# Kernel optimization log

Measured on AMD Instinct MI355X. Metric: run time of the kernel, lower is better.

The kernel has to match this reference:

```python
import jax, jax.numpy as jnp
import numpy as np

B, T, V, C, K = 256, 2048, 128, 512, 10


def setup_inputs() -> dict:
    key = jax.random.key(0)
    k0, k1, k2, k3 = jax.random.split(key, 4)
    x = jax.random.normal(k0, (B, C), dtype=jnp.float32)
    # kappa_old: running attention position, non-negative, somewhere in [0, T)
    kappa_old = jax.random.uniform(k1, (B, K), dtype=jnp.float32) * T
    # onehots: one-hot encoded text, (B, T, V)
    char_ids = jax.random.randint(k2, (B, T), 0, V)
    onehots = jax.nn.one_hot(char_ids, V, dtype=jnp.float32)
    # Linear(cell_size, 3*K) params; torch stores weight as (out, in)
    W = jax.random.normal(k3, (3 * K, C), dtype=jnp.float32) * 0.02
    b = jnp.zeros((3 * K,), dtype=jnp.float32)
    return {"x": x, "kappa_old": kappa_old, "onehots": onehots, "W": W, "b": b}


def reference(x, kappa_old, onehots, W, b):
    max_text_len = onehots.shape[1]
    params = jnp.exp(x @ W.T + b)                      # (B, 3K)
    alpha, beta, pre_kappa = jnp.split(params, 3, axis=-1)  # each (B, K)
    kappa = kappa_old + pre_kappa                      # (B, K)
    indices = jnp.arange(max_text_len, dtype=x.dtype)  # (T,)
    # gravity: (B, K, T) via broadcast, then exp + alpha-weighted reduce over K
    gravity = -beta[:, :, None] * (kappa[:, :, None] - indices) ** 2
    phi = jnp.einsum("bk,bkt->bt", alpha, jnp.exp(gravity))  # (B, T)
    w = jnp.einsum("bt,btv->bv", phi, onehots)               # (B, V)
    return (w, kappa, phi)
```

## Files before the change

kernel.cpp:

```cpp
#include <hip/hip_runtime.h>

#define B_ 256
#define T_ 2048
#define V_ 128
#define C_ 512
#define K_ 10

#define W_OFF 0
#define KAPPA_OFF (B_ * V_)
#define PHI_OFF   (B_ * V_ + B_ * K_)

#define S_ 8
#define TS_ (T_ / S_)

__global__ __launch_bounds__(256) void window_fused(
    const float* __restrict__ x, const float* __restrict__ kappa_old,
    const float* __restrict__ W, const float* __restrict__ bias,
    const float* __restrict__ onehots, float* __restrict__ out) {
  const int s = blockIdx.x;
  const int b = blockIdx.y;
  const int tid = threadIdx.x;

  __shared__ float4 xs4[C_ / 4];
  __shared__ float alpha_s[K_];
  __shared__ float beta_s[K_];
  __shared__ float kap_s[K_];
  __shared__ float phs[TS_];

  if (tid < C_ / 4) xs4[tid] = ((const float4*)(x + b * C_))[tid];
  __syncthreads();

  const int j = tid >> 3;
  const int l = tid & 7;
  if (j < 3 * K_) {
    const float4* Wr = (const float4*)(W + j * C_);
    float4 a4 = make_float4(0.f, 0.f, 0.f, 0.f);
#pragma unroll
    for (int m = 0; m < 16; ++m) {
      const float4 wv = Wr[m * 8 + l];
      const float4 xv = xs4[m * 8 + l];
      a4.x = fmaf(wv.x, xv.x, a4.x);
      a4.y = fmaf(wv.y, xv.y, a4.y);
      a4.z = fmaf(wv.z, xv.z, a4.z);
      a4.w = fmaf(wv.w, xv.w, a4.w);
    }
    float acc = (a4.x + a4.y) + (a4.z + a4.w);
    acc += __shfl_down(acc, 4, 8);
    acc += __shfl_down(acc, 2, 8);
    acc += __shfl_down(acc, 1, 8);
    if (l == 0) {
      const float p = __expf(acc + bias[j]);
      if (j < K_) {
        alpha_s[j] = p;
      } else if (j < 2 * K_) {
        beta_s[j - K_] = p;
      } else {
        const int k = j - 2 * K_;
        const float kk = kappa_old[b * K_ + k] + p;
        kap_s[k] = kk;
        if (s == 0) out[KAPPA_OFF + b * K_ + k] = kk;
      }
    }
  }
  __syncthreads();

  {
    const int t = s * TS_ + tid;
    const float ft = (float)t;
    float ph = 0.0f;
#pragma unroll
    for (int k = 0; k < K_; k++) {
      const float d = kap_s[k] - ft;
      ph += alpha_s[k] * __expf(-beta_s[k] * d * d);
    }
    phs[tid] = ph;
    out[PHI_OFF + b * T_ + t] = ph;
  }
  __syncthreads();

  const int vg = tid & 31;
  const int tr = tid >> 5;
  const float4* base =
      (const float4*)(onehots + ((size_t)b * T_ + (size_t)s * TS_) * V_);

  float4 acc = make_float4(0.f, 0.f, 0.f, 0.f);
#pragma unroll 8
  for (int t = tr; t < TS_; t += 8) {
    const float p = phs[t];
    const float4 o = base[t * (V_ / 4) + vg];
    acc.x = fmaf(p, o.x, acc.x);
    acc.y = fmaf(p, o.y, acc.y);
    acc.z = fmaf(p, o.z, acc.z);
    acc.w = fmaf(p, o.w, acc.w);
  }

  __shared__ float red[8 * V_];
  *(float4*)&red[tr * V_ + vg * 4] = acc;
  __syncthreads();

  if (tid < V_) {
    float s0 = 0.0f;
#pragma unroll
    for (int r = 0; r < 8; r++) s0 += red[r * V_ + tid];
    atomicAdd(&out[W_OFF + b * V_ + tid], s0);
  }
}

extern "C" void kernel_launch(void* const* d_in, const int* in_sizes, int n_in,
                              void* d_out, int out_size, void* d_ws,
                              size_t ws_size, hipStream_t stream) {
  const float* x         = (const float*)d_in[0];
  const float* kappa_old = (const float*)d_in[1];
  const float* onehots   = (const float*)d_in[2];
  const float* W         = (const float*)d_in[3];
  const float* bias      = (const float*)d_in[4];
  float* out = (float*)d_out;

  hipMemsetAsync(d_out, 0, B_ * V_ * sizeof(float), stream);
  window_fused<<<dim3(S_, B_), dim3(256), 0, stream>>>(x, kappa_old, W, bias,
                                                       onehots, out);
}
```

Baseline: 368.2 us.

## Prefetch onehot rows into a register ring before the param matvec

Issues the first eight nontemporal onehot loads per thread before the linear-projection and phi computation, then streams the rest through an 8-deep register ring buffer. The aim is to hide the latency of the memory-bound onehot read behind the matvec and exp work, and to keep the streaming data from polluting the cache. In exchange it holds more registers per thread and relies on the compiler keeping the fully unrolled loop as a software pipeline.

```diff
diff --git a/kernel.cpp b/kernel.cpp
--- a/kernel.cpp
+++ b/kernel.cpp
@@ -12,6 +12,10 @@
 
 #define S_ 8
 #define TS_ (T_ / S_)
+#define RPT 32
+#define PIPE 8
+
+typedef float f4_t __attribute__((ext_vector_type(4)));
 
 __global__ __launch_bounds__(256) void window_fused(
     const float* __restrict__ x, const float* __restrict__ kappa_old,
@@ -21,29 +25,32 @@
   const int b = blockIdx.y;
   const int tid = threadIdx.x;
 
-  __shared__ float4 xs4[C_ / 4];
+  __shared__ f4_t xs4[C_ / 4];
   __shared__ float alpha_s[K_];
   __shared__ float beta_s[K_];
   __shared__ float kap_s[K_];
   __shared__ float phs[TS_];
 
-  if (tid < C_ / 4) xs4[tid] = ((const float4*)(x + b * C_))[tid];
+  const int vg = tid & 31;
+  const int tr = tid >> 5;
+  const f4_t* p0 = (const f4_t*)(onehots +
+                   ((size_t)b * T_ + (size_t)s * TS_ + tr) * V_) + vg;
+
+  f4_t buf[PIPE];
+#pragma unroll
+  for (int i = 0; i < PIPE; ++i)
+    buf[i] = __builtin_nontemporal_load(p0 + i * 256);
+
+  if (tid < C_ / 4) xs4[tid] = ((const f4_t*)(x + b * C_))[tid];
   __syncthreads();
 
   const int j = tid >> 3;
   const int l = tid & 7;
   if (j < 3 * K_) {
-    const float4* Wr = (const float4*)(W + j * C_);
-    float4 a4 = make_float4(0.f, 0.f, 0.f, 0.f);
+    const f4_t* Wr = (const f4_t*)(W + j * C_);
+    f4_t a4 = {0.f, 0.f, 0.f, 0.f};
 #pragma unroll
-    for (int m = 0; m < 16; ++m) {
-      const float4 wv = Wr[m * 8 + l];
-      const float4 xv = xs4[m * 8 + l];
-      a4.x = fmaf(wv.x, xv.x, a4.x);
-      a4.y = fmaf(wv.y, xv.y, a4.y);
-      a4.z = fmaf(wv.z, xv.z, a4.z);
-      a4.w = fmaf(wv.w, xv.w, a4.w);
-    }
+    for (int m = 0; m < 16; ++m) a4 += Wr[m * 8 + l] * xs4[m * 8 + l];
     float acc = (a4.x + a4.y) + (a4.z + a4.w);
     acc += __shfl_down(acc, 4, 8);
     acc += __shfl_down(acc, 2, 8);
@@ -78,24 +85,23 @@
   }
   __syncthreads();
 
-  const int vg = tid & 31;
-  const int tr = tid >> 5;
-  const float4* base =
-      (const float4*)(onehots + ((size_t)b * T_ + (size_t)s * TS_) * V_);
-
-  float4 acc = make_float4(0.f, 0.f, 0.f, 0.f);
-#pragma unroll 8
-  for (int t = tr; t < TS_; t += 8) {
-    const float p = phs[t];
-    const float4 o = base[t * (V_ / 4) + vg];
-    acc.x = fmaf(p, o.x, acc.x);
-    acc.y = fmaf(p, o.y, acc.y);
-    acc.z = fmaf(p, o.z, acc.z);
-    acc.w = fmaf(p, o.w, acc.w);
+  f4_t acc = {0.f, 0.f, 0.f, 0.f};
+#pragma unroll
+  for (int jj = 0; jj < RPT - PIPE; ++jj) {
+    const float p = phs[tr + 8 * jj];
+    const f4_t o = buf[jj & (PIPE - 1)];
+    buf[jj & (PIPE - 1)] =
+        __builtin_nontemporal_load(p0 + (jj + PIPE) * 256);
+    acc += p * o;
+  }
+#pragma unroll
+  for (int jj = RPT - PIPE; jj < RPT; ++jj) {
+    const float p = phs[tr + 8 * jj];
+    acc += p * buf[jj & (PIPE - 1)];
   }
 
   __shared__ float red[8 * V_];
-  *(float4*)&red[tr * V_ + vg * 4] = acc;
+  *(f4_t*)&red[tr * V_ + vg * 4] = acc;
   __syncthreads();
 
   if (tid < V_) {
```

Result: faster. 341.1 us (-7.4%).
